# Performance work log

Measured on AMD Instinct MI355X. Metric: run time of the kernel, lower is better.

The kernel has to match this reference:

```python
import jax, jax.numpy as jnp
import numpy as np
from jax import lax

T, B, I, H = 32768, 1, 128, 512  # seq_len, batch(=1 due to squeeze(1)), input_dim, hidden_dim
HEAD = 25

def setup_inputs() -> dict:
    key = jax.random.key(0)
    ks = jax.random.split(key, 8)
    s = 1.0 / np.sqrt(H)  # pytorch LSTM init scale
    return {
        "x": jax.random.normal(ks[0], (T, B, I), dtype=jnp.float32),
        "W_ih": jax.random.uniform(ks[1], (4 * H, I), jnp.float32, -s, s),
        "W_hh": jax.random.uniform(ks[2], (4 * H, H), jnp.float32, -s, s),
        "b_ih": jax.random.uniform(ks[3], (4 * H,), jnp.float32, -s, s),
        "b_hh": jax.random.uniform(ks[4], (4 * H,), jnp.float32, -s, s),
        "W1": jax.random.uniform(ks[5], (HEAD, H), jnp.float32, -s, s),
        "b1": jax.random.uniform(ks[6], (HEAD,), jnp.float32, -s, s),
        "Wout": jax.random.uniform(ks[7], (1, HEAD), jnp.float32, -s, s),
    }

def reference(x, W_ih, W_hh, b_ih, b_hh, W1, b1, Wout):
    # Precompute input projections for all timesteps (one big GEMM): [T, B, 4H]
    xg = jnp.einsum('tbi,gi->tbg', x, W_ih) + (b_ih + b_hh)

    def step(carry, xg_t):
        h, c = carry  # [B, H] each
        gates = xg_t + h @ W_hh.T  # [B, 4H]
        i_g, f_g, g_g, o_g = jnp.split(gates, 4, axis=-1)  # pytorch gate order i,f,g,o
        i = jax.nn.sigmoid(i_g)
        f = jax.nn.sigmoid(f_g)
        g = jnp.tanh(g_g)
        o = jax.nn.sigmoid(o_g)
        c = f * c + i * g
        h = o * jnp.tanh(c)
        return (h, c), h

    h0 = jnp.zeros((B, H), x.dtype)
    _, hs = lax.scan(step, (h0, h0), xg)  # hs: [T, B, H]

    hid = hs[:, 0, :]  # h_1.squeeze(1) -> [T, H]
    # forward applies c1 then out (c2 is defined but unused in the original)
    out = (hid @ W1.T + b1) @ Wout.T  # [T, 1]
    return out
```

## Files before the change

kernel.cpp:

```cpp
#include <hip/hip_runtime.h>
#include <math.h>


#define T_SEQ 32768
#define HID   512
#define INP   128
#define NWG   32
#define NTH   512
#define HSL   16
#define KW    64
#define KX    16
#define NPK   256

typedef unsigned long long u64;
typedef unsigned int u32;

__device__ __forceinline__ float fast_sigmoid(float x) {
    return 1.0f / (1.0f + __expf(-x));
}
__device__ __forceinline__ float fast_tanh(float x) {
    float a = fabsf(x);
    float e = __expf(-2.0f * a);
    float r = (1.0f - e) / (1.0f + e);
    return copysignf(r, x);
}

__global__ void __launch_bounds__(NTH, 1) lstm_persist(
    const float* __restrict__ x,
    const float* __restrict__ W_ih,
    const float* __restrict__ W_hh,
    const float* __restrict__ b_ih,
    const float* __restrict__ b_hh,
    const float* __restrict__ W1,
    const float* __restrict__ b1,
    const float* __restrict__ Wout,
    u64* __restrict__ hbuf,
    float* __restrict__ out)
{
    const int w   = blockIdx.x;
    const int tid = threadIdx.x;
    const int wv  = tid >> 6;
    const int l   = tid & 63;
    const int rw  = l >> 3;
    const int j   = l & 7;
    const int g   = rw >> 1;
    const int b   = rw & 1;
    const bool is_out = (w == 0 && wv == 1);

    __shared__ __align__(16) float h_lds[2][HID];
    __shared__ u64 gather_lds[8];

    const int grow = g * HID + w * HSL + 2 * wv + b;

    float wr[KW], wi[KX];
#pragma unroll
    for (int kk = 0; kk < 16; ++kk) {
        const int p = (kk + 2 * j) & 15;
        const float4 v4 = *(const float4*)&W_hh[grow * HID + j * KW + 4 * p];
        wr[4 * kk + 0] = v4.x; wr[4 * kk + 1] = v4.y;
        wr[4 * kk + 2] = v4.z; wr[4 * kk + 3] = v4.w;
    }
#pragma unroll
    for (int k = 0; k < KX; k += 4) {
        const float4 v4 = *(const float4*)&W_ih[grow * INP + j * KX + k];
        wi[k] = v4.x; wi[k + 1] = v4.y; wi[k + 2] = v4.z; wi[k + 3] = v4.w;
    }
    float brow = b_ih[grow] + b_hh[grow];

    float weff_o[8];
    float be = 0.0f;
#pragma unroll
    for (int i = 0; i < 8; ++i) weff_o[i] = 0.0f;
    if (is_out) {
#pragma unroll
        for (int i = 0; i < 8; ++i) {
            float s = 0.0f;
            for (int p = 0; p < 25; ++p) s += Wout[p] * W1[p * HID + l + 64 * i];
            weff_o[i] = s;
        }
        for (int p = 0; p < 25; ++p) be += b1[p] * Wout[p];
    }
#pragma unroll
    for (int k = 0; k < KW; ++k) asm volatile("" : "+v"(wr[k]));
#pragma unroll
    for (int k = 0; k < KX; ++k) asm volatile("" : "+v"(wi[k]));
#pragma unroll
    for (int i = 0; i < 8; ++i) asm volatile("" : "+v"(weff_o[i]));
    asm volatile("" : "+v"(brow));
    asm volatile("" : "+v"(be));

    float c = 0.0f;
    float xa[KX];
#pragma unroll
    for (int k = 0; k < KX; ++k) xa[k] = x[j * KX + k];

    bool dead = false;

    for (u32 t = 0; t <= T_SEQ; ++t) {
        if (t == T_SEQ && w != 0) break;

        float xd0 = 0.0f, xd1 = 0.0f, xd2 = 0.0f, xd3 = 0.0f;
#pragma unroll
        for (int k = 0; k < KX; k += 4) {
            xd0 += wi[k + 0] * xa[k + 0];
            xd1 += wi[k + 1] * xa[k + 1];
            xd2 += wi[k + 2] * xa[k + 2];
            xd3 += wi[k + 3] * xa[k + 3];
        }
        const int tn = (t + 1 < T_SEQ) ? (int)(t + 1) : (T_SEQ - 1);
        if (wv != 0) {
#pragma unroll
            for (int k = 0; k < KX; k += 4) {
                const float4 x4 = *(const float4*)&x[tn * INP + j * KX + k];
                xa[k + 0] = x4.x; xa[k + 1] = x4.y;
                xa[k + 2] = x4.z; xa[k + 3] = x4.w;
            }
        }

        if (wv == 0 && !dead) {
            const u64* P = hbuf + (t & 1) * NPK;
            float2* HL = (float2*)h_lds[t & 1];
            bool mine = false;
            int guard = 0;
            while (true) {
                if (!mine) {
                    u64 pr[4];
                    bool ok = true;
#pragma unroll
                    for (int i = 0; i < 4; ++i) {
                        pr[i] = __hip_atomic_load(&P[l + 64 * i],
                                                  __ATOMIC_RELAXED,
                                                  __HIP_MEMORY_SCOPE_AGENT);
                        ok = ok && ((((u32)pr[i]) ^ t) & 15u) == 0u;
                    }
                    if (ok) {
#pragma unroll
                        for (int i = 0; i < 4; ++i) {
                            float2 hp;
                            hp.x = __uint_as_float((u32)pr[i]);
                            hp.y = __uint_as_float((u32)(pr[i] >> 32));
                            HL[l + 64 * i] = hp;
                        }
                        mine = true;
                    }
                }
                if (__ballot(mine) == ~0ull) break;
                if (++guard > (1 << 22)) { dead = true; break; }
            }
        }
        __syncthreads();

        if (t < T_SEQ) {
            float a0 = xd0, a1 = xd1, a2 = xd2, a3 = xd3;
            const float4* hl4 = (const float4*)&h_lds[t & 1][j * KW];
#pragma unroll
            for (int kk = 0; kk < 16; ++kk) {
                const int p = (kk + 2 * j) & 15;
                const float4 h4 = hl4[p];
                a0 += wr[4 * kk + 0] * h4.x;
                a1 += wr[4 * kk + 1] * h4.y;
                a2 += wr[4 * kk + 2] * h4.z;
                a3 += wr[4 * kk + 3] * h4.w;
            }
            if (wv == 0) {
#pragma unroll
                for (int k = 0; k < KX; k += 4) {
                    const float4 x4 = *(const float4*)&x[tn * INP + j * KX + k];
                    xa[k + 0] = x4.x; xa[k + 1] = x4.y;
                    xa[k + 2] = x4.z; xa[k + 3] = x4.w;
                }
            }
            float acc = (a0 + a1) + (a2 + a3);
            acc += __shfl_xor(acc, 1);
            acc += __shfl_xor(acc, 2);
            acc += __shfl_xor(acc, 4);
            acc += brow;
            const float ig = acc;
            const float fg = __shfl(acc, l + 16);
            const float gg = __shfl(acc, l + 32);
            const float og = __shfl(acc, l + 48);
            const float iv = fast_sigmoid(ig);
            const float fv = fast_sigmoid(fg);
            const float gv = fast_tanh(gg);
            const float ov = fast_sigmoid(og);
            c = fv * c + iv * gv;
            const float hv = ov * fast_tanh(c);
            const float hv1 = __shfl(hv, 8);
            if (l == 0) {
                const u32 b0 = (__float_as_uint(hv) & ~15u) | ((t + 1) & 15u);
                const u32 b1v = __float_as_uint(hv1);
                gather_lds[wv] = ((u64)b1v << 32) | (u64)b0;
            }
            __syncthreads();
            if (wv == 0 && l < 8) {
                __hip_atomic_store(&hbuf[((t + 1) & 1) * NPK + w * 8 + l],
                                   gather_lds[l],
                                   __ATOMIC_RELAXED, __HIP_MEMORY_SCOPE_AGENT);
            }
        }

        if (is_out && t >= 1) {
            float pd = 0.0f;
#pragma unroll
            for (int i = 0; i < 8; ++i)
                pd += h_lds[t & 1][l + 64 * i] * weff_o[i];
            pd += __shfl_xor(pd, 1);
            pd += __shfl_xor(pd, 2);
            pd += __shfl_xor(pd, 4);
            pd += __shfl_xor(pd, 8);
            pd += __shfl_xor(pd, 16);
            pd += __shfl_xor(pd, 32);
            if (l == 0) out[t - 1] = pd + be;
        }
    }
}

extern "C" void kernel_launch(void* const* d_in, const int* in_sizes, int n_in,
                              void* d_out, int out_size, void* d_ws, size_t ws_size,
                              hipStream_t stream)
{
    const float* x    = (const float*)d_in[0];
    const float* W_ih = (const float*)d_in[1];
    const float* W_hh = (const float*)d_in[2];
    const float* b_ih = (const float*)d_in[3];
    const float* b_hh = (const float*)d_in[4];
    const float* W1   = (const float*)d_in[5];
    const float* b1   = (const float*)d_in[6];
    const float* Wout = (const float*)d_in[7];
    float* out = (float*)d_out;

    u64* hbuf = (u64*)d_ws;

    hipMemsetAsync(d_ws, 0, 2 * NPK * sizeof(u64), stream);
    lstm_persist<<<NWG, NTH, 0, stream>>>(x, W_ih, W_hh, b_ih, b_hh, W1, b1,
                                          Wout, hbuf, out);
}
```

Baseline: 65.57 ms.

## Spread workgroups across XCDs and poll h-state via sc0 loads with slow fallback

The kernel launches 256 blocks but keeps only every eighth, so the 32 active workgroups land one per XCD slot under round-robin dispatch. The h-state exchange polls a fast buffer with raw sc0 global loads, falling back to agent-scope atomic loads on a duplicate buffer once a step spins too long. The tag grows to 8 bits by also tagging the second float, which makes stale-data checks stronger. The aim is lower latency for the cross-workgroup step barrier, at the cost of double stores, a reliance on hardware placement, and a reliance on the coherence behaviour of sc0 loads.

```diff
diff --git a/kernel.cpp b/kernel.cpp
--- a/kernel.cpp
+++ b/kernel.cpp
@@ -6,6 +6,7 @@
 #define HID   512
 #define INP   128
 #define NWG   32
+#define GRID  256
 #define NTH   512
 #define HSL   16
 #define KW    64
@@ -34,10 +35,13 @@
     const float* __restrict__ W1,
     const float* __restrict__ b1,
     const float* __restrict__ Wout,
-    u64* __restrict__ hbuf,
+    u64* __restrict__ hb_fast,
+    u64* __restrict__ hb_slow,
     float* __restrict__ out)
 {
-    const int w   = blockIdx.x;
+    const int bid = blockIdx.x;
+    if (bid & 7) return;
+    const int w   = bid >> 3;
     const int tid = threadIdx.x;
     const int wv  = tid >> 6;
     const int l   = tid & 63;
@@ -95,6 +99,8 @@
     for (int k = 0; k < KX; ++k) xa[k] = x[j * KX + k];
 
     bool dead = false;
+    bool slowMode = false;
+    int  slowSteps = 0;
 
     for (u32 t = 0; t <= T_SEQ; ++t) {
         if (t == T_SEQ && w != 0) break;
@@ -118,34 +124,84 @@
         }
 
         if (wv == 0 && !dead) {
-            const u64* P = hbuf + (t & 1) * NPK;
             float2* HL = (float2*)h_lds[t & 1];
-            bool mine = false;
-            int guard = 0;
-            while (true) {
-                if (!mine) {
-                    u64 pr[4];
-                    bool ok = true;
-#pragma unroll
-                    for (int i = 0; i < 4; ++i) {
-                        pr[i] = __hip_atomic_load(&P[l + 64 * i],
-                                                  __ATOMIC_RELAXED,
-                                                  __HIP_MEMORY_SCOPE_AGENT);
-                        ok = ok && ((((u32)pr[i]) ^ t) & 15u) == 0u;
+            if (t == 0) {
+                float2 z; z.x = 0.0f; z.y = 0.0f;
+                HL[l +   0] = z;
+                HL[l +  64] = z;
+                HL[l + 128] = z;
+                HL[l + 192] = z;
+            } else {
+                const int par = (t & 1) * NPK;
+                const u64 a0 = (u64)(hb_fast + par + l);
+                const u64 a1 = a0 +  64u * sizeof(u64);
+                const u64 a2 = a0 + 128u * sizeof(u64);
+                const u64 a3 = a0 + 192u * sizeof(u64);
+                const u64* PS = hb_slow + par;
+                const u32 tLo = t & 15u;
+                const u32 tHi = (t >> 4) & 15u;
+                const int ft = (t < 4) ? 4096 : 96;
+                bool mine = false;
+                bool slow = slowMode;
+                int it = 0;
+                while (true) {
+                    if (!mine) {
+                        u64 p0, p1, p2, p3;
+                        if (!slow) {
+                            asm volatile(
+                                "global_load_dwordx2 %0, %4, off sc0\n\t"
+                                "global_load_dwordx2 %1, %5, off sc0\n\t"
+                                "global_load_dwordx2 %2, %6, off sc0\n\t"
+                                "global_load_dwordx2 %3, %7, off sc0\n\t"
+                                "s_waitcnt vmcnt(0)"
+                                : "=&v"(p0), "=&v"(p1), "=&v"(p2), "=&v"(p3)
+                                : "v"(a0), "v"(a1), "v"(a2), "v"(a3)
+                                : "memory");
+                            __builtin_amdgcn_sched_barrier(0);
+                        } else {
+                            p0 = __hip_atomic_load(PS + l, __ATOMIC_RELAXED,
+                                                   __HIP_MEMORY_SCOPE_AGENT);
+                            p1 = __hip_atomic_load(PS + l + 64, __ATOMIC_RELAXED,
+                                                   __HIP_MEMORY_SCOPE_AGENT);
+                            p2 = __hip_atomic_load(PS + l + 128, __ATOMIC_RELAXED,
+                                                   __HIP_MEMORY_SCOPE_AGENT);
+                            p3 = __hip_atomic_load(PS + l + 192, __ATOMIC_RELAXED,
+                                                   __HIP_MEMORY_SCOPE_AGENT);
+                        }
+                        const bool ok =
+                            ((((u32)p0 ^ tLo) & 15u) == 0u) &&
+                            ((((u32)(p0 >> 32) ^ tHi) & 15u) == 0u) &&
+                            ((((u32)p1 ^ tLo) & 15u) == 0u) &&
+                            ((((u32)(p1 >> 32) ^ tHi) & 15u) == 0u) &&
+                            ((((u32)p2 ^ tLo) & 15u) == 0u) &&
+                            ((((u32)(p2 >> 32) ^ tHi) & 15u) == 0u) &&
+                            ((((u32)p3 ^ tLo) & 15u) == 0u) &&
+                            ((((u32)(p3 >> 32) ^ tHi) & 15u) == 0u);
+                        if (ok) {
+                            float2 h0, h1, h2, h3;
+                            h0.x = __uint_as_float((u32)p0);
+                            h0.y = __uint_as_float((u32)(p0 >> 32));
+                            h1.x = __uint_as_float((u32)p1);
+                            h1.y = __uint_as_float((u32)(p1 >> 32));
+                            h2.x = __uint_as_float((u32)p2);
+                            h2.y = __uint_as_float((u32)(p2 >> 32));
+                            h3.x = __uint_as_float((u32)p3);
+                            h3.y = __uint_as_float((u32)(p3 >> 32));
+                            HL[l +   0] = h0;
+                            HL[l +  64] = h1;
+                            HL[l + 128] = h2;
+                            HL[l + 192] = h3;
+                            mine = true;
+                        }
                     }
-                    if (ok) {
-#pragma unroll
-                        for (int i = 0; i < 4; ++i) {
-                            float2 hp;
-                            hp.x = __uint_as_float((u32)pr[i]);
-                            hp.y = __uint_as_float((u32)(pr[i] >> 32));
-                            HL[l + 64 * i] = hp;
-                        }
-                        mine = true;
-                    }
+                    if (__ballot(mine) == ~0ull) break;
+                    ++it;
+                    if (it == ft) slow = true;
+                    if (it > (1 << 22)) { dead = true; break; }
                 }
-                if (__ballot(mine) == ~0ull) break;
-                if (++guard > (1 << 22)) { dead = true; break; }
+                if (slow && !slowMode && t >= 4) {
+                    if (++slowSteps >= 3) slowMode = true;
+                }
             }
         }
         __syncthreads();
@@ -187,14 +243,18 @@
             const float hv = ov * fast_tanh(c);
             const float hv1 = __shfl(hv, 8);
             if (l == 0) {
-                const u32 b0 = (__float_as_uint(hv) & ~15u) | ((t + 1) & 15u);
-                const u32 b1v = __float_as_uint(hv1);
+                const u32 b0  = (__float_as_uint(hv)  & ~15u) | ((t + 1) & 15u);
+                const u32 b1v = (__float_as_uint(hv1) & ~15u) | (((t + 1) >> 4) & 15u);
                 gather_lds[wv] = ((u64)b1v << 32) | (u64)b0;
             }
             __syncthreads();
             if (wv == 0 && l < 8) {
-                __hip_atomic_store(&hbuf[((t + 1) & 1) * NPK + w * 8 + l],
-                                   gather_lds[l],
+                const u64 pkt = gather_lds[l];
+                const int idx = ((t + 1) & 1) * NPK + w * 8 + l;
+                const u64 adf = (u64)&hb_fast[idx];
+                asm volatile("global_store_dwordx2 %0, %1, off"
+                             :: "v"(adf), "v"(pkt) : "memory");
+                __hip_atomic_store(&hb_slow[idx], pkt,
                                    __ATOMIC_RELAXED, __HIP_MEMORY_SCOPE_AGENT);
             }
         }
@@ -229,9 +289,10 @@
     const float* Wout = (const float*)d_in[7];
     float* out = (float*)d_out;
 
-    u64* hbuf = (u64*)d_ws;
-
-    hipMemsetAsync(d_ws, 0, 2 * NPK * sizeof(u64), stream);
-    lstm_persist<<<NWG, NTH, 0, stream>>>(x, W_ih, W_hh, b_ih, b_hh, W1, b1,
-                                          Wout, hbuf, out);
-}
+    u64* hb_fast = (u64*)d_ws;
+    u64* hb_slow = hb_fast + 2 * NPK;
+
+    hipMemsetAsync(d_ws, 0, 4 * NPK * sizeof(u64), stream);
+    lstm_persist<<<GRID, NTH, 0, stream>>>(x, W_ih, W_hh, b_ih, b_hh, W1, b1,
+                                           Wout, hb_fast, hb_slow, out);
+}
```

Measured after the change: 73.80 ms. +12.6%, slower.

## Pipeline cross-workgroup h polling with double-buffered inline-asm loads and rotate publisher wave

Applied to the files above, without the earlier changes.

Replaces the simple atomic-load spin loop that gathers the hidden state from all workgroups with a hand-written polling scheme. It keeps two sets of cache-bypassing global loads in flight, checks one while the other is outstanding, and falls back to the old atomic spin after repeated misses. It also tags both halves of each packet with an 8-bit step tag, zero-fills h at step 0 instead of polling, and rotates which wave publishes the packet so the store is not issued by the polling wave. This aims to cut per-step inter-workgroup synchronization latency, at the cost of more complex inline asm and wait-count assumptions, plus one more mantissa bit of h overwritten by the tag.

```diff
diff --git a/kernel.cpp b/kernel.cpp
--- a/kernel.cpp
+++ b/kernel.cpp
@@ -11,6 +11,7 @@
 #define KW    64
 #define KX    16
 #define NPK   256
+#define FT    48
 
 typedef unsigned long long u64;
 typedef unsigned int u32;
@@ -95,6 +96,11 @@
     for (int k = 0; k < KX; ++k) xa[k] = x[j * KX + k];
 
     bool dead = false;
+    bool slowMode = false;
+    int  slowSteps = 0;
+
+#define TAGOK(p) (((((u32)(p)) ^ tLo) & 15u) == 0u && \
+                  ((((u32)((p) >> 32)) ^ tHi) & 15u) == 0u)
 
     for (u32 t = 0; t <= T_SEQ; ++t) {
         if (t == T_SEQ && w != 0) break;
@@ -118,34 +124,113 @@
         }
 
         if (wv == 0 && !dead) {
-            const u64* P = hbuf + (t & 1) * NPK;
             float2* HL = (float2*)h_lds[t & 1];
-            bool mine = false;
-            int guard = 0;
-            while (true) {
-                if (!mine) {
-                    u64 pr[4];
-                    bool ok = true;
-#pragma unroll
-                    for (int i = 0; i < 4; ++i) {
-                        pr[i] = __hip_atomic_load(&P[l + 64 * i],
-                                                  __ATOMIC_RELAXED,
-                                                  __HIP_MEMORY_SCOPE_AGENT);
-                        ok = ok && ((((u32)pr[i]) ^ t) & 15u) == 0u;
+            if (t == 0) {
+                float2 z; z.x = 0.0f; z.y = 0.0f;
+                HL[l +   0] = z;
+                HL[l +  64] = z;
+                HL[l + 128] = z;
+                HL[l + 192] = z;
+            } else {
+                const u64* P = hbuf + (t & 1) * NPK;
+                const u64 a0 = (u64)(P + l);
+                const u64 a1 = a0 +  64u * sizeof(u64);
+                const u64 a2 = a0 + 128u * sizeof(u64);
+                const u64 a3 = a0 + 192u * sizeof(u64);
+                const u32 tLo = t & 15u;
+                const u32 tHi = (t >> 4) & 15u;
+                u64 r0 = 0, r1 = 0, r2 = 0, r3 = 0;
+                bool got = false;
+
+                if (!slowMode) {
+                    u64 qa0, qa1, qa2, qa3, qb0, qb1, qb2, qb3;
+                    asm volatile(
+                        "global_load_dwordx2 %0, %4, off sc0 sc1\n\t"
+                        "global_load_dwordx2 %1, %5, off sc0 sc1\n\t"
+                        "global_load_dwordx2 %2, %6, off sc0 sc1\n\t"
+                        "global_load_dwordx2 %3, %7, off sc0 sc1"
+                        : "=&v"(qa0), "=&v"(qa1), "=&v"(qa2), "=&v"(qa3)
+                        : "v"(a0), "v"(a1), "v"(a2), "v"(a3) : "memory");
+                    asm volatile(
+                        "global_load_dwordx2 %0, %4, off sc0 sc1\n\t"
+                        "global_load_dwordx2 %1, %5, off sc0 sc1\n\t"
+                        "global_load_dwordx2 %2, %6, off sc0 sc1\n\t"
+                        "global_load_dwordx2 %3, %7, off sc0 sc1"
+                        : "=&v"(qb0), "=&v"(qb1), "=&v"(qb2), "=&v"(qb3)
+                        : "v"(a0), "v"(a1), "v"(a2), "v"(a3) : "memory");
+                    int it = 0;
+                    while (true) {
+                        asm volatile("s_waitcnt vmcnt(4)" ::: "memory");
+                        __builtin_amdgcn_sched_barrier(0);
+                        bool ok = TAGOK(qa0) && TAGOK(qa1) &&
+                                  TAGOK(qa2) && TAGOK(qa3);
+                        if (__ballot(ok) == ~0ull) {
+                            r0 = qa0; r1 = qa1; r2 = qa2; r3 = qa3;
+                            got = true; break;
+                        }
+                        asm volatile(
+                            "global_load_dwordx2 %0, %4, off sc0 sc1\n\t"
+                            "global_load_dwordx2 %1, %5, off sc0 sc1\n\t"
+                            "global_load_dwordx2 %2, %6, off sc0 sc1\n\t"
+                            "global_load_dwordx2 %3, %7, off sc0 sc1"
+                            : "=&v"(qa0), "=&v"(qa1), "=&v"(qa2), "=&v"(qa3)
+                            : "v"(a0), "v"(a1), "v"(a2), "v"(a3) : "memory");
+                        if (++it > FT) break;
+                        asm volatile("s_waitcnt vmcnt(4)" ::: "memory");
+                        __builtin_amdgcn_sched_barrier(0);
+                        ok = TAGOK(qb0) && TAGOK(qb1) &&
+                             TAGOK(qb2) && TAGOK(qb3);
+                        if (__ballot(ok) == ~0ull) {
+                            r0 = qb0; r1 = qb1; r2 = qb2; r3 = qb3;
+                            got = true; break;
+                        }
+                        asm volatile(
+                            "global_load_dwordx2 %0, %4, off sc0 sc1\n\t"
+                            "global_load_dwordx2 %1, %5, off sc0 sc1\n\t"
+                            "global_load_dwordx2 %2, %6, off sc0 sc1\n\t"
+                            "global_load_dwordx2 %3, %7, off sc0 sc1"
+                            : "=&v"(qb0), "=&v"(qb1), "=&v"(qb2), "=&v"(qb3)
+                            : "v"(a0), "v"(a1), "v"(a2), "v"(a3) : "memory");
+                        if (++it > FT) break;
                     }
-                    if (ok) {
-#pragma unroll
-                        for (int i = 0; i < 4; ++i) {
-                            float2 hp;
-                            hp.x = __uint_as_float((u32)pr[i]);
-                            hp.y = __uint_as_float((u32)(pr[i] >> 32));
-                            HL[l + 64 * i] = hp;
-                        }
-                        mine = true;
+                    if (!got && t >= 4) {
+                        if (++slowSteps >= 8) slowMode = true;
                     }
                 }
-                if (__ballot(mine) == ~0ull) break;
-                if (++guard > (1 << 22)) { dead = true; break; }
+                if (!got) {
+                    asm volatile("s_waitcnt vmcnt(0)" ::: "memory");
+                    __builtin_amdgcn_sched_barrier(0);
+                    int guard = 0;
+                    while (true) {
+                        r0 = __hip_atomic_load(P + l, __ATOMIC_RELAXED,
+                                               __HIP_MEMORY_SCOPE_AGENT);
+                        r1 = __hip_atomic_load(P + l + 64, __ATOMIC_RELAXED,
+                                               __HIP_MEMORY_SCOPE_AGENT);
+                        r2 = __hip_atomic_load(P + l + 128, __ATOMIC_RELAXED,
+                                               __HIP_MEMORY_SCOPE_AGENT);
+                        r3 = __hip_atomic_load(P + l + 192, __ATOMIC_RELAXED,
+                                               __HIP_MEMORY_SCOPE_AGENT);
+                        const bool ok = TAGOK(r0) && TAGOK(r1) &&
+                                        TAGOK(r2) && TAGOK(r3);
+                        if (__ballot(ok) == ~0ull) break;
+                        if (++guard > (1 << 22)) { dead = true; break; }
+                    }
+                }
+                {
+                    float2 h0, h1, h2, h3;
+                    h0.x = __uint_as_float((u32)r0);
+                    h0.y = __uint_as_float((u32)(r0 >> 32));
+                    h1.x = __uint_as_float((u32)r1);
+                    h1.y = __uint_as_float((u32)(r1 >> 32));
+                    h2.x = __uint_as_float((u32)r2);
+                    h2.y = __uint_as_float((u32)(r2 >> 32));
+                    h3.x = __uint_as_float((u32)r3);
+                    h3.y = __uint_as_float((u32)(r3 >> 32));
+                    HL[l +   0] = h0;
+                    HL[l +  64] = h1;
+                    HL[l + 128] = h2;
+                    HL[l + 192] = h3;
+                }
             }
         }
         __syncthreads();
@@ -187,15 +272,17 @@
             const float hv = ov * fast_tanh(c);
             const float hv1 = __shfl(hv, 8);
             if (l == 0) {
-                const u32 b0 = (__float_as_uint(hv) & ~15u) | ((t + 1) & 15u);
-                const u32 b1v = __float_as_uint(hv1);
+                const u32 b0  = (__float_as_uint(hv)  & ~15u) | ((t + 1) & 15u);
+                const u32 b1v = (__float_as_uint(hv1) & ~15u) | (((t + 1) >> 4) & 15u);
                 gather_lds[wv] = ((u64)b1v << 32) | (u64)b0;
             }
             __syncthreads();
-            if (wv == 0 && l < 8) {
+            const int mwv = 2 + (int)(t % 6u);
+            if (wv == mwv && l < 8) {
+                const u64 pkt = gather_lds[l];
                 __hip_atomic_store(&hbuf[((t + 1) & 1) * NPK + w * 8 + l],
-                                   gather_lds[l],
-                                   __ATOMIC_RELAXED, __HIP_MEMORY_SCOPE_AGENT);
+                                   pkt, __ATOMIC_RELAXED,
+                                   __HIP_MEMORY_SCOPE_AGENT);
             }
         }
 
@@ -213,6 +300,7 @@
             if (l == 0) out[t - 1] = pd + be;
         }
     }
+#undef TAGOK
 }
 
 extern "C" void kernel_launch(void* const* d_in, const int* in_sizes, int n_in,
```

After: 76.98 ms. +17.4%, slower.
